# Performance work log

Hardware: AMD Instinct MI355X
Metric: run time of the kernel (lower is better)

The kernel has to match this reference:

```python
import jax, jax.numpy as jnp
import numpy as np

H = 16  # num_heads (matches init_kwargs)


def setup_inputs() -> dict:
    key = jax.random.key(0)
    ks = jax.random.split(key, 5)
    B, T, C = 4, 2048, 2048
    S = C // H
    g = 0.5 * (6.0 / (C + C)) ** 0.5 * (3.0 ** 0.5)  # ~xavier_uniform scale, gain 0.5
    x = jax.random.normal(ks[0], (B, T, C), dtype=jnp.float32)
    Wk = jax.random.uniform(ks[1], (C, C), jnp.float32, -g, g)
    Wv = jax.random.uniform(ks[2], (C, C), jnp.float32, -g, g)
    Wr = jax.random.uniform(ks[3], (C, C), jnp.float32, -g, g)
    Wo = jax.random.uniform(ks[4], (C, C), jnp.float32, -g, g)
    time_decay = jnp.full((H, S), -5.0, dtype=jnp.float32)
    time_first = jnp.zeros((H, S), dtype=jnp.float32)
    return {"x": x, "Wk": Wk, "Wv": Wv, "Wr": Wr, "Wo": Wo,
            "time_decay": time_decay, "time_first": time_first}


def _wkv(k, v, time_decay, time_first):
    # k, v: [B, T, H, S] float32
    decay = jnp.exp(-jnp.exp(time_decay.astype(jnp.float32)))  # [H, S]
    first = jnp.exp(time_first.astype(jnp.float32))            # [H, S]
    w = jnp.exp(jnp.clip(k.astype(jnp.float32), -10.0, 10.0))  # [B, T, H, S]
    # t==0 branch (state = first*w0*v0) == uniform recurrence with w0 scaled by first
    w = w.at[:, 0].multiply(first)
    wt = jnp.swapaxes(w, 0, 1)                    # [T, B, H, S]
    vt = jnp.swapaxes(v.astype(jnp.float32), 0, 1)

    def step(carry, inp):
        num, den = carry
        w_t, v_t = inp
        num = decay * num + w_t * v_t
        den = decay * den + w_t
        return (num, den), num / (den + 1e-6)

    B, _, _, S = k.shape
    init = (jnp.zeros((B, H, S), jnp.float32), jnp.zeros((B, H, S), jnp.float32))
    _, wkv = jax.lax.scan(step, init, (wt, vt))   # [T, B, H, S]
    return jnp.swapaxes(wkv, 0, 1).astype(k.dtype)  # [B, T, H, S]


def reference(x, Wk, Wv, Wr, Wo, time_decay, time_first):
    B, T, C = x.shape
    S = C // H
    k = (x @ Wk.T).reshape(B, T, H, S)
    v = (x @ Wv.T).reshape(B, T, H, S)
    r = (x @ Wr.T).reshape(B, T, H, S)
    wkv = _wkv(k, v, time_decay, time_first)
    rwkv = (jax.nn.sigmoid(r) * wkv).reshape(B, T, C)
    return rwkv @ Wo.T
```

## Files before the change

### kernel.cpp

```cpp
#include <hip/hip_runtime.h>
#include <hip/hip_bf16.h>

using bf16 = __hip_bfloat16;
using floatx4 = __attribute__((ext_vector_type(4))) float;
using bf16x8  = __attribute__((ext_vector_type(8))) __bf16;
using bf16x2  = __attribute__((ext_vector_type(2))) __bf16;

#define MDIM 8192
#define NDIM 2048
#define KDIM 2048
#define TSEQ 2048
#define BB   4
#define CDIM 2048
#define NCHUNK 64
#define TCHUNK 32

typedef __attribute__((address_space(1))) void gvoid_t;
typedef __attribute__((address_space(3))) void lvoid_t;

__device__ __forceinline__ void load_lds16(const void* g, void* l) {
  __builtin_amdgcn_global_load_lds((gvoid_t*)(void*)g, (lvoid_t*)l, 16, 0, 0);
}

__global__ __launch_bounds__(256) void cvt_all(
    const float* __restrict__ x,
    const float* __restrict__ Wk, const float* __restrict__ Wv,
    const float* __restrict__ Wr, const float* __restrict__ Wo,
    __bf16* __restrict__ xb,
    __bf16* __restrict__ wkb, __bf16* __restrict__ wvb,
    __bf16* __restrict__ wrb, __bf16* __restrict__ wob) {
  const size_t WN = (size_t)NDIM * KDIM;
  const int slice = blockIdx.y;
  const float* s;
  __bf16* d;
  if (slice < 4) { s = x + (size_t)slice * WN; d = xb + (size_t)slice * WN; }
  else {
    s = (slice == 4) ? Wk : (slice == 5) ? Wv : (slice == 6) ? Wr : Wo;
    d = (slice == 4) ? wkb : (slice == 5) ? wvb : (slice == 6) ? wrb : wob;
  }
  const int i = (blockIdx.x * 256 + threadIdx.x) * 8;
  float4 a = *(const float4*)(s + i);
  float4 b = *(const float4*)(s + i + 4);
  bf16x8 o;
  o[0] = (__bf16)a.x; o[1] = (__bf16)a.y; o[2] = (__bf16)a.z; o[3] = (__bf16)a.w;
  o[4] = (__bf16)b.x; o[5] = (__bf16)b.y; o[6] = (__bf16)b.z; o[7] = (__bf16)b.w;
  *(bf16x8*)(d + i) = o;
}


#define GBARRIER() asm volatile("s_barrier" ::: "memory")
#define VMW4()     asm volatile("s_waitcnt vmcnt(4)" ::: "memory")
#define VMW0()     asm volatile("s_waitcnt vmcnt(0)" ::: "memory")

template <typename CT>
__device__ __forceinline__ void gemm256_body(const __bf16* __restrict__ A,
                                             const __bf16* __restrict__ B,
                                             CT* __restrict__ C,
                                             const int bm, const int bn) {
  __shared__ __attribute__((aligned(128))) unsigned char lds[131072];
  const int tid  = threadIdx.x;
  const int lane = tid & 63;
  const int wave = tid >> 6;
  const int wm = wave >> 2;
  const int wn = wave & 3;

  floatx4 acc[8][4] = {};
  bf16x8 af[8], bfr[2];

  const int srow = tid >> 2;
  const int scol = ((tid & 3) ^ ((tid >> 3) & 3)) * 8;
  const __bf16* Ag = A + (size_t)(bm * 256 + srow) * KDIM + scol;
  const __bf16* Bg = B + (size_t)(bn * 256 + srow) * KDIM + scol;
  const uint32_t sdst = (uint32_t)tid * 16u;

  const uint32_t laneoff =
      (uint32_t)((lane & 15) * 64 + (((lane >> 4) ^ ((lane >> 1) & 3)) * 16));
  const uint32_t aoff = (uint32_t)(wm * 8192) + laneoff;
  const uint32_t boff = 65536u +
      (uint32_t)((wn >> 1) * 8192 + (wn & 1) * 4096) + laneoff;

#define STG_A(bf_, kt_, kk_, rh_)                                             \
  load_lds16(Ag + (size_t)(rh_) * 128 * KDIM + (size_t)((kt_) * 64 + (kk_) * 32), \
             (void*)(lds + (bf_) + (kk_) * 16384u + (rh_) * 8192u + sdst))
#define STG_B(bf_, kt_, kk_, rh_)                                             \
  load_lds16(Bg + (size_t)(rh_) * 128 * KDIM + (size_t)((kt_) * 64 + (kk_) * 32), \
             (void*)(lds + 65536u + (bf_) + (kk_) * 16384u + (rh_) * 8192u + sdst))
#define RD_A(kk_, bo_) {                                                      \
  const uint32_t ab = (bo_) + (kk_) * 16384u + aoff;                          \
  af[0] = *(const bf16x8*)(lds + ab);        af[1] = *(const bf16x8*)(lds + ab + 1024); \
  af[2] = *(const bf16x8*)(lds + ab + 2048); af[3] = *(const bf16x8*)(lds + ab + 3072); \
  af[4] = *(const bf16x8*)(lds + ab + 4096); af[5] = *(const bf16x8*)(lds + ab + 5120); \
  af[6] = *(const bf16x8*)(lds + ab + 6144); af[7] = *(const bf16x8*)(lds + ab + 7168); }
#define RD_B(kk_, n0_, bo_) {                                                 \
  const uint32_t bb = (bo_) + (kk_) * 16384u + boff + (n0_) * 1024u;          \
  bfr[0] = *(const bf16x8*)(lds + bb);                                        \
  bfr[1] = *(const bf16x8*)(lds + bb + 1024); }
#define MFMA8(j0_, j1_) {                                                     \
  __builtin_amdgcn_s_setprio(1);                                              \
  _Pragma("unroll")                                                           \
  for (int m_ = 0; m_ < 8; ++m_) {                                            \
    acc[m_][j0_] = __builtin_amdgcn_mfma_f32_16x16x32_bf16(af[m_], bfr[0], acc[m_][j0_], 0, 0, 0); \
    acc[m_][j1_] = __builtin_amdgcn_mfma_f32_16x16x32_bf16(af[m_], bfr[1], acc[m_][j1_], 0, 0, 0); \
  }                                                                           \
  __builtin_amdgcn_s_setprio(0); }

  STG_A(0u, 0, 0, 0); STG_A(0u, 0, 0, 1);
  STG_B(0u, 0, 0, 0); STG_B(0u, 0, 0, 1);
  STG_A(0u, 0, 1, 0); STG_A(0u, 0, 1, 1);
  STG_B(0u, 0, 1, 0); STG_B(0u, 0, 1, 1);
  VMW4();
  GBARRIER();

  constexpr int NT = KDIM / 64;
  for (int t = 0; t < NT - 1; ++t) {
    const uint32_t bo  = (uint32_t)(t & 1) * 32768u;
    const uint32_t bo1 = bo ^ 32768u;
    RD_A(0, bo); RD_B(0, 0, bo);
    STG_A(bo1, t + 1, 0, 0); STG_A(bo1, t + 1, 0, 1);
    GBARRIER();
    MFMA8(0, 1);
    GBARRIER();
    RD_B(0, 2, bo);
    STG_B(bo1, t + 1, 0, 0); STG_B(bo1, t + 1, 0, 1);
    VMW4();
    GBARRIER();
    MFMA8(2, 3);
    GBARRIER();
    RD_A(1, bo); RD_B(1, 0, bo);
    STG_A(bo1, t + 1, 1, 0); STG_A(bo1, t + 1, 1, 1);
    GBARRIER();
    MFMA8(0, 1);
    GBARRIER();
    RD_B(1, 2, bo);
    STG_B(bo1, t + 1, 1, 0); STG_B(bo1, t + 1, 1, 1);
    VMW4();
    GBARRIER();
    MFMA8(2, 3);
    GBARRIER();
  }
  {
    const uint32_t bo = (uint32_t)((NT - 1) & 1) * 32768u;
    RD_A(0, bo); RD_B(0, 0, bo);
    GBARRIER();
    MFMA8(0, 1);
    GBARRIER();
    RD_B(0, 2, bo);
    VMW0();
    GBARRIER();
    MFMA8(2, 3);
    GBARRIER();
    RD_A(1, bo); RD_B(1, 0, bo);
    MFMA8(0, 1);
    RD_B(1, 2, bo);
    MFMA8(2, 3);
  }

  const int crow = (lane >> 4) * 4;
  const int ccol = lane & 15;
#pragma unroll
  for (int i = 0; i < 8; ++i)
#pragma unroll
    for (int j = 0; j < 4; ++j) {
      const size_t r0 = (size_t)(bm * 256 + wm * 128 + i * 16 + crow);
      const int    c0 = bn * 256 + wn * 64 + j * 16 + ccol;
#pragma unroll
      for (int rg = 0; rg < 4; ++rg)
        C[(r0 + rg) * NDIM + c0] = (CT)(acc[i][j][rg]);
    }
#undef STG_A
#undef STG_B
#undef RD_A
#undef RD_B
#undef MFMA8
}

__device__ __forceinline__ void xcd_swz(int& bm, int& bn) {
  const int f = (int)(blockIdx.y * 32 + blockIdx.x);
  const int s = (f & 7) * 32 + (f >> 3);
  bm = s & 31;
  bn = s >> 5;
}

__global__ __launch_bounds__(512, 2) void gemm_qkv(const __bf16* __restrict__ x,
                                                   const __bf16* __restrict__ Wk,
                                                   const __bf16* __restrict__ Wv,
                                                   const __bf16* __restrict__ Wr,
                                                   __bf16* __restrict__ kb,
                                                   __bf16* __restrict__ vb,
                                                   __bf16* __restrict__ rb) {
  const __bf16* Bsel = (blockIdx.z == 0) ? Wk : (blockIdx.z == 1) ? Wv : Wr;
  __bf16*       Csel = (blockIdx.z == 0) ? kb : (blockIdx.z == 1) ? vb : rb;
  int bm, bn; xcd_swz(bm, bn);
  gemm256_body<__bf16>(x, Bsel, Csel, bm, bn);
}

__global__ __launch_bounds__(512, 2) void gemm_o(const __bf16* __restrict__ A,
                                                 const __bf16* __restrict__ B,
                                                 float* __restrict__ C) {
  int bm, bn; xcd_swz(bm, bn);
  gemm256_body<float>(A, B, C, bm, bn);
}

__global__ __launch_bounds__(256) void wkv_summary(
    const __bf16* __restrict__ kb, const __bf16* __restrict__ vb,
    const float* __restrict__ td, const float* __restrict__ tf,
    float* __restrict__ nsum, float* __restrict__ dsum) {
  const int c0 = (blockIdx.x * 256 + threadIdx.x) * 2;
  const int chunk = blockIdx.y;
  const int b = blockIdx.z;
  const float dc0 = __expf(-__expf(td[c0]));
  const float dc1 = __expf(-__expf(td[c0 + 1]));
  const float fi0 = __expf(tf[c0]);
  const float fi1 = __expf(tf[c0 + 1]);
  size_t base = ((size_t)b * TSEQ + (size_t)chunk * TCHUNK) * CDIM + c0;
  float n0 = 0.f, d0 = 0.f, n1 = 0.f, d1 = 0.f;
#pragma unroll 4
  for (int t = 0; t < TCHUNK; ++t) {
    bf16x2 k2 = *(const bf16x2*)(kb + base + (size_t)t * CDIM);
    bf16x2 v2 = *(const bf16x2*)(vb + base + (size_t)t * CDIM);
    float k0f = fminf(fmaxf((float)k2[0], -10.f), 10.f);
    float k1f = fminf(fmaxf((float)k2[1], -10.f), 10.f);
    float w0 = __expf(k0f), w1 = __expf(k1f);
    if (chunk == 0 && t == 0) { w0 *= fi0; w1 *= fi1; }
    n0 = dc0 * n0 + w0 * (float)v2[0];
    d0 = dc0 * d0 + w0;
    n1 = dc1 * n1 + w1 * (float)v2[1];
    d1 = dc1 * d1 + w1;
  }
  const size_t si = (size_t)(chunk * BB + b) * CDIM + c0;
  *(float2*)(nsum + si) = make_float2(n0, n1);
  *(float2*)(dsum + si) = make_float2(d0, d1);
}

__global__ __launch_bounds__(256) void wkv_scan(
    const float* __restrict__ td,
    float* __restrict__ nsum, float* __restrict__ dsum) {
  const int c0 = (blockIdx.x * 256 + threadIdx.x) * 2;
  const int b = blockIdx.y;
  const float dT0 = __expf(-__expf(td[c0]) * (float)TCHUNK);
  const float dT1 = __expf(-__expf(td[c0 + 1]) * (float)TCHUNK);
  float pn0 = 0.f, pd0 = 0.f, pn1 = 0.f, pd1 = 0.f;
  for (int j = 0; j < NCHUNK; ++j) {
    const size_t si = (size_t)(j * BB + b) * CDIM + c0;
    float2 Sn = *(const float2*)(nsum + si);
    float2 Sd = *(const float2*)(dsum + si);
    *(float2*)(nsum + si) = make_float2(pn0, pn1);
    *(float2*)(dsum + si) = make_float2(pd0, pd1);
    pn0 = dT0 * pn0 + Sn.x;  pn1 = dT1 * pn1 + Sn.y;
    pd0 = dT0 * pd0 + Sd.x;  pd1 = dT1 * pd1 + Sd.y;
  }
}

__global__ __launch_bounds__(256) void wkv_apply(
    const __bf16* __restrict__ kb, const __bf16* __restrict__ vb,
    __bf16* __restrict__ rb,
    const float* __restrict__ td, const float* __restrict__ tf,
    const float* __restrict__ nsum, const float* __restrict__ dsum) {
  const int c0 = (blockIdx.x * 256 + threadIdx.x) * 2;
  const int chunk = blockIdx.y;
  const int b = blockIdx.z;
  const float dc0 = __expf(-__expf(td[c0]));
  const float dc1 = __expf(-__expf(td[c0 + 1]));
  const float fi0 = __expf(tf[c0]);
  const float fi1 = __expf(tf[c0 + 1]);

  const size_t si = (size_t)(chunk * BB + b) * CDIM + c0;
  float2 pn = *(const float2*)(nsum + si);
  float2 pd = *(const float2*)(dsum + si);
  float n0 = pn.x, n1 = pn.y, d0 = pd.x, d1 = pd.y;

  size_t base = ((size_t)b * TSEQ + (size_t)chunk * TCHUNK) * CDIM + c0;
#pragma unroll 2
  for (int t = 0; t < TCHUNK; ++t) {
    const size_t idx = base + (size_t)t * CDIM;
    bf16x2 k2 = *(const bf16x2*)(kb + idx);
    bf16x2 v2 = *(const bf16x2*)(vb + idx);
    bf16x2 r2 = *(const bf16x2*)(rb + idx);
    float k0f = fminf(fmaxf((float)k2[0], -10.f), 10.f);
    float k1f = fminf(fmaxf((float)k2[1], -10.f), 10.f);
    float w0 = __expf(k0f), w1 = __expf(k1f);
    if (chunk == 0 && t == 0) { w0 *= fi0; w1 *= fi1; }
    n0 = dc0 * n0 + w0 * (float)v2[0];
    d0 = dc0 * d0 + w0;
    n1 = dc1 * n1 + w1 * (float)v2[1];
    d1 = dc1 * d1 + w1;
    const float wkv0 = n0 * __builtin_amdgcn_rcpf(d0 + 1e-6f);
    const float wkv1 = n1 * __builtin_amdgcn_rcpf(d1 + 1e-6f);
    const float sr0 = __builtin_amdgcn_rcpf(1.f + __expf(-(float)r2[0]));
    const float sr1 = __builtin_amdgcn_rcpf(1.f + __expf(-(float)r2[1]));
    bf16x2 o;
    o[0] = (__bf16)(sr0 * wkv0);
    o[1] = (__bf16)(sr1 * wkv1);
    *(bf16x2*)(rb + idx) = o;
  }
}

extern "C" void kernel_launch(void* const* d_in, const int* in_sizes, int n_in,
                              void* d_out, int out_size, void* d_ws, size_t ws_size,
                              hipStream_t stream) {
  const float* x  = (const float*)d_in[0];
  const float* Wk = (const float*)d_in[1];
  const float* Wv = (const float*)d_in[2];
  const float* Wr = (const float*)d_in[3];
  const float* Wo = (const float*)d_in[4];
  const float* td = (const float*)d_in[5];
  const float* tf = (const float*)d_in[6];
  float* out = (float*)d_out;

  char* ws = (char*)d_ws;
  const size_t matX = (size_t)MDIM * KDIM * sizeof(__bf16);
  const size_t matW = (size_t)NDIM * KDIM * sizeof(__bf16);
  __bf16* xb  = (__bf16*)(ws);
  __bf16* wkb = (__bf16*)(ws + matX);
  __bf16* wvb = (__bf16*)(ws + matX + matW);
  __bf16* wrb = (__bf16*)(ws + matX + 2 * matW);
  __bf16* wob = (__bf16*)(ws + matX + 3 * matW);
  __bf16* kb  = (__bf16*)(ws + matX + 4 * matW);
  __bf16* vb  = (__bf16*)(ws + 2 * matX + 4 * matW);
  __bf16* rb  = (__bf16*)(ws + 3 * matX + 4 * matW);
  float* nsum = (float*)(ws + 4 * matX + 4 * matW);
  float* dsum = nsum + (size_t)NCHUNK * BB * CDIM;

  dim3 blk(256);
  dim3 blk5(512);
  cvt_all<<<dim3(NDIM * KDIM / (8 * 256), 8), blk, 0, stream>>>(
      x, Wk, Wv, Wr, Wo, xb, wkb, wvb, wrb, wob);

  dim3 gq(MDIM / 256, NDIM / 256, 3);
  gemm_qkv<<<gq, blk5, 0, stream>>>(xb, wkb, wvb, wrb, kb, vb, rb);
  dim3 gw(CDIM / 512, NCHUNK, BB);
  wkv_summary<<<gw, blk, 0, stream>>>(kb, vb, td, tf, nsum, dsum);
  wkv_scan<<<dim3(CDIM / 512, BB), blk, 0, stream>>>(td, nsum, dsum);
  wkv_apply<<<gw, blk, 0, stream>>>(kb, vb, rb, td, tf, nsum, dsum);
  dim3 go(MDIM / 256, NDIM / 256, 1);
  gemm_o<<<go, blk5, 0, stream>>>(rb, wob, out);
}
```

Baseline: 466.5 us.

## Restructure GEMM inner loop into 4x4 MFMA sub-tiles with deeper K prefetch

Changes the register fragment split from 8 A by 2 B to 4 A by 4 B, so each MFMA group issues 16 MMAs over a square sub-tile with fewer LDS reads per MFMA. The global-to-LDS staging is regrouped by K-half and issued further ahead, prefetching part of tile t+2 into the buffer being drained, with waits loosened to vmcnt(8). This aims to hide global-load latency and cut LDS read traffic. The price is more in-flight loads and a more delicate buffer-reuse ordering that relies on the barriers being placed correctly.

Result: slower. 481.9 us (+3.3%).

```diff
diff --git a/kernel.cpp b/kernel.cpp
--- a/kernel.cpp
+++ b/kernel.cpp
@@ -49,6 +49,7 @@
 
 
 #define GBARRIER() asm volatile("s_barrier" ::: "memory")
+#define VMW8()     asm volatile("s_waitcnt vmcnt(8)" ::: "memory")
 #define VMW4()     asm volatile("s_waitcnt vmcnt(4)" ::: "memory")
 #define VMW0()     asm volatile("s_waitcnt vmcnt(0)" ::: "memory")
 
@@ -65,7 +66,7 @@
   const int wn = wave & 3;
 
   floatx4 acc[8][4] = {};
-  bf16x8 af[8], bfr[2];
+  bf16x8 af[4], bfr[4];
 
   const int srow = tid >> 2;
   const int scol = ((tid & 3) ^ ((tid >> 3) & 3)) * 8;
@@ -85,74 +86,94 @@
 #define STG_B(bf_, kt_, kk_, rh_)                                             \
   load_lds16(Bg + (size_t)(rh_) * 128 * KDIM + (size_t)((kt_) * 64 + (kk_) * 32), \
              (void*)(lds + 65536u + (bf_) + (kk_) * 16384u + (rh_) * 8192u + sdst))
-#define RD_A(kk_, bo_) {                                                      \
-  const uint32_t ab = (bo_) + (kk_) * 16384u + aoff;                          \
+#define STG_KH(bf_, kt_, kk_) {                                               \
+  STG_A(bf_, kt_, kk_, 0); STG_A(bf_, kt_, kk_, 1);                           \
+  STG_B(bf_, kt_, kk_, 0); STG_B(bf_, kt_, kk_, 1); }
+#define RD_A(kk_, mh_, bo_) {                                                 \
+  const uint32_t ab = (bo_) + (kk_) * 16384u + (mh_) * 4096u + aoff;          \
   af[0] = *(const bf16x8*)(lds + ab);        af[1] = *(const bf16x8*)(lds + ab + 1024); \
-  af[2] = *(const bf16x8*)(lds + ab + 2048); af[3] = *(const bf16x8*)(lds + ab + 3072); \
-  af[4] = *(const bf16x8*)(lds + ab + 4096); af[5] = *(const bf16x8*)(lds + ab + 5120); \
-  af[6] = *(const bf16x8*)(lds + ab + 6144); af[7] = *(const bf16x8*)(lds + ab + 7168); }
-#define RD_B(kk_, n0_, bo_) {                                                 \
-  const uint32_t bb = (bo_) + (kk_) * 16384u + boff + (n0_) * 1024u;          \
-  bfr[0] = *(const bf16x8*)(lds + bb);                                        \
-  bfr[1] = *(const bf16x8*)(lds + bb + 1024); }
-#define MFMA8(j0_, j1_) {                                                     \
+  af[2] = *(const bf16x8*)(lds + ab + 2048); af[3] = *(const bf16x8*)(lds + ab + 3072); }
+#define RD_B(kk_, bo_) {                                                      \
+  const uint32_t bb = (bo_) + (kk_) * 16384u + boff;                          \
+  bfr[0] = *(const bf16x8*)(lds + bb);        bfr[1] = *(const bf16x8*)(lds + bb + 1024); \
+  bfr[2] = *(const bf16x8*)(lds + bb + 2048); bfr[3] = *(const bf16x8*)(lds + bb + 3072); }
+#define MFMA16(mh_) {                                                         \
   __builtin_amdgcn_s_setprio(1);                                              \
   _Pragma("unroll")                                                           \
-  for (int m_ = 0; m_ < 8; ++m_) {                                            \
-    acc[m_][j0_] = __builtin_amdgcn_mfma_f32_16x16x32_bf16(af[m_], bfr[0], acc[m_][j0_], 0, 0, 0); \
-    acc[m_][j1_] = __builtin_amdgcn_mfma_f32_16x16x32_bf16(af[m_], bfr[1], acc[m_][j1_], 0, 0, 0); \
+  for (int i_ = 0; i_ < 4; ++i_) {                                            \
+    _Pragma("unroll")                                                         \
+    for (int j_ = 0; j_ < 4; ++j_)                                            \
+      acc[(mh_) * 4 + i_][j_] = __builtin_amdgcn_mfma_f32_16x16x32_bf16(      \
+          af[i_], bfr[j_], acc[(mh_) * 4 + i_][j_], 0, 0, 0);                 \
   }                                                                           \
   __builtin_amdgcn_s_setprio(0); }
 
-  STG_A(0u, 0, 0, 0); STG_A(0u, 0, 0, 1);
-  STG_B(0u, 0, 0, 0); STG_B(0u, 0, 0, 1);
-  STG_A(0u, 0, 1, 0); STG_A(0u, 0, 1, 1);
-  STG_B(0u, 0, 1, 0); STG_B(0u, 0, 1, 1);
-  VMW4();
+  STG_KH(0u, 0, 0);
+  STG_KH(0u, 0, 1);
+  STG_KH(32768u, 1, 0);
+  VMW8();
   GBARRIER();
 
   constexpr int NT = KDIM / 64;
-  for (int t = 0; t < NT - 1; ++t) {
+  for (int t = 0; t < NT - 2; ++t) {
     const uint32_t bo  = (uint32_t)(t & 1) * 32768u;
     const uint32_t bo1 = bo ^ 32768u;
-    RD_A(0, bo); RD_B(0, 0, bo);
-    STG_A(bo1, t + 1, 0, 0); STG_A(bo1, t + 1, 0, 1);
-    GBARRIER();
-    MFMA8(0, 1);
-    GBARRIER();
-    RD_B(0, 2, bo);
-    STG_B(bo1, t + 1, 0, 0); STG_B(bo1, t + 1, 0, 1);
+    RD_A(0, 0, bo); RD_B(0, bo);
+    STG_KH(bo1, t + 1, 1);
+    GBARRIER();
+    MFMA16(0);
+    GBARRIER();
+    RD_A(0, 1, bo);
+    VMW8();
+    GBARRIER();
+    MFMA16(1);
+    GBARRIER();
+    RD_A(1, 0, bo); RD_B(1, bo);
+    GBARRIER();
+    MFMA16(0);
+    GBARRIER();
+    RD_A(1, 1, bo);
+    STG_KH(bo, t + 2, 0);
+    VMW8();
+    GBARRIER();
+    MFMA16(1);
+    GBARRIER();
+  }
+  {
+    const uint32_t bo  = (uint32_t)((NT - 2) & 1) * 32768u;
+    const uint32_t bo1 = bo ^ 32768u;
+    RD_A(0, 0, bo); RD_B(0, bo);
+    STG_KH(bo1, NT - 1, 1);
+    GBARRIER();
+    MFMA16(0);
+    GBARRIER();
+    RD_A(0, 1, bo);
+    VMW8();
+    GBARRIER();
+    MFMA16(1);
+    GBARRIER();
+    RD_A(1, 0, bo); RD_B(1, bo);
+    GBARRIER();
+    MFMA16(0);
+    GBARRIER();
+    RD_A(1, 1, bo);
     VMW4();
     GBARRIER();
-    MFMA8(2, 3);
-    GBARRIER();
-    RD_A(1, bo); RD_B(1, 0, bo);
-    STG_A(bo1, t + 1, 1, 0); STG_A(bo1, t + 1, 1, 1);
-    GBARRIER();
-    MFMA8(0, 1);
-    GBARRIER();
-    RD_B(1, 2, bo);
-    STG_B(bo1, t + 1, 1, 0); STG_B(bo1, t + 1, 1, 1);
-    VMW4();
-    GBARRIER();
-    MFMA8(2, 3);
+    MFMA16(1);
     GBARRIER();
   }
   {
     const uint32_t bo = (uint32_t)((NT - 1) & 1) * 32768u;
-    RD_A(0, bo); RD_B(0, 0, bo);
-    GBARRIER();
-    MFMA8(0, 1);
-    GBARRIER();
-    RD_B(0, 2, bo);
+    RD_A(0, 0, bo); RD_B(0, bo);
+    MFMA16(0);
+    RD_A(0, 1, bo);
+    MFMA16(1);
     VMW0();
     GBARRIER();
-    MFMA8(2, 3);
-    GBARRIER();
-    RD_A(1, bo); RD_B(1, 0, bo);
-    MFMA8(0, 1);
-    RD_B(1, 2, bo);
-    MFMA8(2, 3);
+    RD_A(1, 0, bo); RD_B(1, bo);
+    MFMA16(0);
+    RD_A(1, 1, bo);
+    MFMA16(1);
   }
 
   const int crow = (lane >> 4) * 4;
@@ -169,9 +190,10 @@
     }
 #undef STG_A
 #undef STG_B
+#undef STG_KH
 #undef RD_A
 #undef RD_B
-#undef MFMA8
+#undef MFMA16
 }
 
 __device__ __forceinline__ void xcd_swz(int& bm, int& bn) {
```

## Restructure GEMM mainloop to K=32 stages with 4-buffer, 3-deep prefetch

Applied to the files above, without the earlier changes.

The 256x256 bf16 GEMM mainloop moves from double-buffered K=64 tiles to four LDS buffers of K=32 tiles, keeping three stages of global-to-LDS loads in flight and waiting with vmcnt(8). The aim is to hide global memory latency better by prefetching further ahead while the total LDS footprint stays at 128KB. Each iteration now carries two barrier pairs per 32-wide K step, the same ratio as before, and the epilogue is split into three drain stages. There is a risk that the changed wait counts or the buffer reuse distance introduce hazards, or that the extra loop iterations add overhead.

Measured after the change: 468.4 us. Within noise of the previous version (+0.4%).

```diff
diff --git a/kernel.cpp b/kernel.cpp
--- a/kernel.cpp
+++ b/kernel.cpp
@@ -49,6 +49,7 @@
 
 
 #define GBARRIER() asm volatile("s_barrier" ::: "memory")
+#define VMW8()     asm volatile("s_waitcnt vmcnt(8)" ::: "memory")
 #define VMW4()     asm volatile("s_waitcnt vmcnt(4)" ::: "memory")
 #define VMW0()     asm volatile("s_waitcnt vmcnt(0)" ::: "memory")
 
@@ -76,83 +77,89 @@
   const uint32_t laneoff =
       (uint32_t)((lane & 15) * 64 + (((lane >> 4) ^ ((lane >> 1) & 3)) * 16));
   const uint32_t aoff = (uint32_t)(wm * 8192) + laneoff;
-  const uint32_t boff = 65536u +
-      (uint32_t)((wn >> 1) * 8192 + (wn & 1) * 4096) + laneoff;
-
-#define STG_A(bf_, kt_, kk_, rh_)                                             \
-  load_lds16(Ag + (size_t)(rh_) * 128 * KDIM + (size_t)((kt_) * 64 + (kk_) * 32), \
-             (void*)(lds + (bf_) + (kk_) * 16384u + (rh_) * 8192u + sdst))
-#define STG_B(bf_, kt_, kk_, rh_)                                             \
-  load_lds16(Bg + (size_t)(rh_) * 128 * KDIM + (size_t)((kt_) * 64 + (kk_) * 32), \
-             (void*)(lds + 65536u + (bf_) + (kk_) * 16384u + (rh_) * 8192u + sdst))
-#define RD_A(kk_, bo_) {                                                      \
-  const uint32_t ab = (bo_) + (kk_) * 16384u + aoff;                          \
+  const uint32_t boff = 16384u + (uint32_t)(wn * 4096) + laneoff;
+
+#define BUF(t_) ((uint32_t)((t_) & 3) * 32768u)
+#define STG_A(t_) {                                                           \
+  load_lds16(Ag + (size_t)(t_) * 32,                                          \
+             (void*)(lds + BUF(t_) + sdst));                                  \
+  load_lds16(Ag + (size_t)128 * KDIM + (size_t)(t_) * 32,                     \
+             (void*)(lds + BUF(t_) + 8192u + sdst)); }
+#define STG_B(t_) {                                                           \
+  load_lds16(Bg + (size_t)(t_) * 32,                                          \
+             (void*)(lds + BUF(t_) + 16384u + sdst));                         \
+  load_lds16(Bg + (size_t)128 * KDIM + (size_t)(t_) * 32,                     \
+             (void*)(lds + BUF(t_) + 24576u + sdst)); }
+#define RD_AF(bo_) {                                                          \
+  const uint32_t ab = (bo_) + aoff;                                           \
   af[0] = *(const bf16x8*)(lds + ab);        af[1] = *(const bf16x8*)(lds + ab + 1024); \
   af[2] = *(const bf16x8*)(lds + ab + 2048); af[3] = *(const bf16x8*)(lds + ab + 3072); \
   af[4] = *(const bf16x8*)(lds + ab + 4096); af[5] = *(const bf16x8*)(lds + ab + 5120); \
   af[6] = *(const bf16x8*)(lds + ab + 6144); af[7] = *(const bf16x8*)(lds + ab + 7168); }
-#define RD_B(kk_, n0_, bo_) {                                                 \
-  const uint32_t bb = (bo_) + (kk_) * 16384u + boff + (n0_) * 1024u;          \
+#define RD_BF(bo_, nh_) {                                                     \
+  const uint32_t bb = (bo_) + boff + (nh_) * 2048u;                           \
   bfr[0] = *(const bf16x8*)(lds + bb);                                        \
   bfr[1] = *(const bf16x8*)(lds + bb + 1024); }
-#define MFMA8(j0_, j1_) {                                                     \
+#define MFMA16(j0_) {                                                         \
   __builtin_amdgcn_s_setprio(1);                                              \
   _Pragma("unroll")                                                           \
   for (int m_ = 0; m_ < 8; ++m_) {                                            \
-    acc[m_][j0_] = __builtin_amdgcn_mfma_f32_16x16x32_bf16(af[m_], bfr[0], acc[m_][j0_], 0, 0, 0); \
-    acc[m_][j1_] = __builtin_amdgcn_mfma_f32_16x16x32_bf16(af[m_], bfr[1], acc[m_][j1_], 0, 0, 0); \
+    acc[m_][(j0_)]     = __builtin_amdgcn_mfma_f32_16x16x32_bf16(af[m_], bfr[0], acc[m_][(j0_)], 0, 0, 0);     \
+    acc[m_][(j0_) + 1] = __builtin_amdgcn_mfma_f32_16x16x32_bf16(af[m_], bfr[1], acc[m_][(j0_) + 1], 0, 0, 0); \
   }                                                                           \
   __builtin_amdgcn_s_setprio(0); }
 
-  STG_A(0u, 0, 0, 0); STG_A(0u, 0, 0, 1);
-  STG_B(0u, 0, 0, 0); STG_B(0u, 0, 0, 1);
-  STG_A(0u, 0, 1, 0); STG_A(0u, 0, 1, 1);
-  STG_B(0u, 0, 1, 0); STG_B(0u, 0, 1, 1);
-  VMW4();
+  STG_A(0); STG_B(0);
+  STG_A(1); STG_B(1);
+  STG_A(2); STG_B(2);
+  VMW8();
   GBARRIER();
 
-  constexpr int NT = KDIM / 64;
-  for (int t = 0; t < NT - 1; ++t) {
-    const uint32_t bo  = (uint32_t)(t & 1) * 32768u;
-    const uint32_t bo1 = bo ^ 32768u;
-    RD_A(0, bo); RD_B(0, 0, bo);
-    STG_A(bo1, t + 1, 0, 0); STG_A(bo1, t + 1, 0, 1);
-    GBARRIER();
-    MFMA8(0, 1);
-    GBARRIER();
-    RD_B(0, 2, bo);
-    STG_B(bo1, t + 1, 0, 0); STG_B(bo1, t + 1, 0, 1);
+  constexpr int NT = KDIM / 32;
+  for (int t = 0; t < NT - 3; ++t) {
+    const uint32_t bo = BUF(t);
+    RD_AF(bo); RD_BF(bo, 0);
+    STG_A(t + 3);
+    GBARRIER();
+    MFMA16(0);
+    GBARRIER();
+    RD_BF(bo, 1);
+    STG_B(t + 3);
+    VMW8();
+    GBARRIER();
+    MFMA16(2);
+    GBARRIER();
+  }
+  {
+    const uint32_t bo = BUF(NT - 3);
+    RD_AF(bo); RD_BF(bo, 0);
+    GBARRIER();
+    MFMA16(0);
+    GBARRIER();
+    RD_BF(bo, 1);
     VMW4();
     GBARRIER();
-    MFMA8(2, 3);
-    GBARRIER();
-    RD_A(1, bo); RD_B(1, 0, bo);
-    STG_A(bo1, t + 1, 1, 0); STG_A(bo1, t + 1, 1, 1);
-    GBARRIER();
-    MFMA8(0, 1);
-    GBARRIER();
-    RD_B(1, 2, bo);
-    STG_B(bo1, t + 1, 1, 0); STG_B(bo1, t + 1, 1, 1);
-    VMW4();
-    GBARRIER();
-    MFMA8(2, 3);
+    MFMA16(2);
     GBARRIER();
   }
   {
-    const uint32_t bo = (uint32_t)((NT - 1) & 1) * 32768u;
-    RD_A(0, bo); RD_B(0, 0, bo);
-    GBARRIER();
-    MFMA8(0, 1);
-    GBARRIER();
-    RD_B(0, 2, bo);
+    const uint32_t bo = BUF(NT - 2);
+    RD_AF(bo); RD_BF(bo, 0);
+    GBARRIER();
+    MFMA16(0);
+    GBARRIER();
+    RD_BF(bo, 1);
     VMW0();
     GBARRIER();
-    MFMA8(2, 3);
-    GBARRIER();
-    RD_A(1, bo); RD_B(1, 0, bo);
-    MFMA8(0, 1);
-    RD_B(1, 2, bo);
-    MFMA8(2, 3);
+    MFMA16(2);
+    GBARRIER();
+  }
+  {
+    const uint32_t bo = BUF(NT - 1);
+    RD_AF(bo); RD_BF(bo, 0);
+    MFMA16(0);
+    RD_BF(bo, 1);
+    MFMA16(2);
   }
 
   const int crow = (lane >> 4) * 4;
@@ -167,11 +174,12 @@
       for (int rg = 0; rg < 4; ++rg)
         C[(r0 + rg) * NDIM + c0] = (CT)(acc[i][j][rg]);
     }
+#undef BUF
 #undef STG_A
 #undef STG_B
-#undef RD_A
-#undef RD_B
-#undef MFMA8
+#undef RD_AF
+#undef RD_BF
+#undef MFMA16
 }
 
 __device__ __forceinline__ void xcd_swz(int& bm, int& bn) {
```
